# Performance work log

Hardware: AMD Instinct MI355X
Metric: run time of the kernel (lower is better)

The kernel has to match this reference:

```python
import jax, jax.numpy as jnp
import numpy as np

B, C, H, W = 8, 3, 512, 512
KH = KW = 17          # blur kernel
F_REG, D = 24, 4      # regularization filters, Wiener filters
RKH = RKW = 5         # reg-filter kernel size


def psf2otf(psf, shape):
    """Zero-pad psf to `shape`, circshift so center is at (0,0), FFT."""
    kh, kw = psf.shape[-2:]
    Ho, Wo = shape
    pad = [(0, 0)] * (psf.ndim - 2) + [(0, Ho - kh), (0, Wo - kw)]
    p = jnp.pad(psf, pad)
    p = jnp.roll(p, (-(kh // 2), -(kw // 2)), axis=(-2, -1))
    return jnp.fft.fft2(p)


def edgetaper(img, psf):
    """MATLAB-style edgetaper. img: (C,Hp,Wp), psf: (kh,kw)."""
    Ho, Wo = img.shape[-2:]

    def autocorr(proj, n):
        z = jnp.zeros((n,), img.dtype).at[: proj.shape[0]].set(proj)
        z = jnp.fft.ifft(jnp.abs(jnp.fft.fft(z)) ** 2).real
        z = jnp.concatenate([z, z[:1]])  # length n+1
        return z / z.max()

    beta0 = autocorr(psf.sum(1), Ho - 1)  # (Ho,)
    beta1 = autocorr(psf.sum(0), Wo - 1)  # (Wo,)
    alpha = (1.0 - beta0)[:, None] * (1.0 - beta1)[None, :]  # (Ho,Wo)
    blurred = jnp.fft.ifft2(jnp.fft.fft2(img) * psf2otf(psf, (Ho, Wo))).real
    return alpha * img + (1.0 - alpha) * blurred


def wiener_one(y, psf, g, log_alpha):
    """Multi-filter Wiener deconvolution for one image.
    y: (C,Hp,Wp), psf: (kh,kw), g: (F,1,rkh,rkw), log_alpha: (D,1).
    Returns (D,C,Hp,Wp)."""
    Ho, Wo = y.shape[-2:]
    K = psf2otf(psf, (Ho, Wo))                  # (Hp,Wp) complex
    G = psf2otf(g[:, 0], (Ho, Wo))              # (F,Hp,Wp)
    Greg = jnp.sum(jnp.abs(G) ** 2, axis=0)     # (Hp,Wp)
    Y = jnp.fft.fft2(y)                         # (C,Hp,Wp)
    a = jnp.exp(log_alpha)[:, :, None, None]    # (D,1,1,1)
    S = jnp.abs(K) ** 2 + a * Greg              # (D,1,Hp,Wp)
    X = (jnp.conj(K) * Y)[None] / S             # (D,C,Hp,Wp)
    return jnp.fft.ifft2(X).real


def forward(image, blurKernel, stdn, wiener_conv_weights, wiener_scale, alpha, weights):
    kh, kw = blurKernel.shape[-2:]
    # getPad2RetainShape
    pt, pb = (kh + 1) // 2 - 1, kh - (kh + 1) // 2
    pl, pr = (kw + 1) // 2 - 1, kw - (kw + 1) // 2
    x = jnp.pad(image, ((0, 0), (0, 0), (pt, pb), (pl, pr)), mode='symmetric')
    psf = blurKernel[:, 0]                      # (B,kh,kw)
    x = jax.vmap(edgetaper)(x, psf)             # (B,C,Hp,Wp)
    # WeightNormalization: zero-mean then L2-normalize per filter, times scale
    w = wiener_conv_weights - wiener_conv_weights.mean(axis=(1, 2, 3), keepdims=True)
    nrm = jnp.sqrt(jnp.sum(w * w, axis=(1, 2, 3), keepdims=True))
    w = w * (wiener_scale.reshape(-1, 1, 1, 1) / nrm)
    xw = jax.vmap(lambda yi, ki: wiener_one(yi, ki, w, alpha))(x, psf)  # (B,D,C,Hp,Wp)
    Hp, Wp = x.shape[-2:]
    crop = xw[..., pt:Hp - pb, pl:Wp - pr]      # Crop2D back to (H,W)
    return jnp.sum(crop * weights, axis=1)      # weighted mix over D -> (B,C,H,W)


def setup_inputs() -> dict:
    key = jax.random.key(0)
    ks = jax.random.split(key, 4)
    image = jax.random.uniform(ks[0], (B, C, H, W), jnp.float32)
    k = jax.random.uniform(ks[1], (B, 1, KH, KW), jnp.float32)
    blurKernel = k / jnp.sum(k, axis=(-2, -1), keepdims=True)  # normalized psf
    stdn = jax.random.uniform(ks[2], (B,), jnp.float32) * 0.05 + 0.01
    wiener_conv_weights = jax.random.normal(ks[3], (F_REG, 1, RKH, RKW), jnp.float32)
    wiener_scale = jnp.full((F_REG,), 0.1, jnp.float32)
    alpha = jnp.log(jnp.logspace(np.log10(1e-3), np.log10(1e-1), D))[:, None].astype(jnp.float32)
    weights = jnp.full((1, D, 1, 1, 1), 1.0 / D, jnp.float32)
    return {"image": image, "blurKernel": blurKernel, "stdn": stdn,
            "wiener_conv_weights": wiener_conv_weights, "wiener_scale": wiener_scale,
            "alpha": alpha, "weights": weights}


def reference(image, blurKernel, stdn, wiener_conv_weights, wiener_scale, alpha, weights):
    return forward(image, blurKernel, stdn, wiener_conv_weights, wiener_scale, alpha, weights)
```

## Files before the change

kernel.cpp:

```cpp
#include <hip/hip_runtime.h>
#include <hip/hip_bf16.h>

#define NN 528
#define NP (NN*NN)
#define IMG 512
#define IMGP (IMG*IMG)
#define PAD 8
#define KH 17
#define KT (KH*KH)
#define NF 24
#define RK 5
#define RKT (RK*RK)
#define ND 4
#define TOPB (17*NN)
#define ROWB (2*TOPB)
#define SIDEB (494*34)
#define BORD (ROWB + SIDEB)
#define AST 34

static __device__ __forceinline__ float ldx(const void* p, long i, int bf) {
    if (bf) return __bfloat162float(((const __hip_bfloat16*)p)[i]);
    return ((const float*)p)[i];
}

static __device__ __forceinline__ int gmap(int m) {
    if (m < -8)  return 495 - m;
    if (m < 0)   return -m - 1;
    if (m < 512) return m;
    if (m < 520) return 1023 - m;
    return 527 - m;
}

static __device__ __forceinline__ void s1_pair(const float2* __restrict__ X,
                                               float2* __restrict__ A,
                                               const float2* __restrict__ TW,
                                               const float2* __restrict__ T33,
                                               float s, int task) {
    int k2 = task >> 3, n1h = task & 7, n1 = n1h << 1;
    const float4* Xv = (const float4*)X;
    float a0r = 0.f, a0i = 0.f, a1r = 0.f, a1i = 0.f;
    int m = 0;
    for (int n2 = 0; n2 < 33; ++n2) {
        float4 xv = Xv[n1h + 8*n2];
        float2 w = T33[m]; m += k2; if (m >= 33) m -= 33;
        float wr = w.x, wi = s*w.y;
        a0r += xv.x*wr - xv.y*wi; a0i += xv.x*wi + xv.y*wr;
        a1r += xv.z*wr - xv.w*wi; a1i += xv.z*wi + xv.w*wr;
    }
    float2 t0 = TW[n1*k2], t1 = TW[(n1+1)*k2];
    float t0r = t0.x, t0i = s*t0.y, t1r = t1.x, t1i = s*t1.y;
    A[n1*AST + k2]     = make_float2(a0r*t0r - a0i*t0i, a0r*t0i + a0i*t0r);
    A[(n1+1)*AST + k2] = make_float2(a1r*t1r - a1i*t1i, a1r*t1i + a1i*t1r);
}

static __device__ __forceinline__ void s2_pair(const float2* __restrict__ A,
                                               const float2* __restrict__ T16,
                                               float s, int task,
                                               int* o0, float2* y0, int* o1, float2* y1) {
    int k1 = task / 17, kp = task - 17*k1;
    if (kp < 16) {
        int k2 = kp << 1;
        const float4* Av = (const float4*)A;
        float a0r = 0.f, a0i = 0.f, a1r = 0.f, a1i = 0.f;
        int m = 0;
        for (int n1 = 0; n1 < 16; ++n1) {
            float4 av = Av[(n1*AST + k2) >> 1];
            float2 w = T16[m]; m = (m + k1) & 15;
            float wr = w.x, wi = s*w.y;
            a0r += av.x*wr - av.y*wi; a0i += av.x*wi + av.y*wr;
            a1r += av.z*wr - av.w*wi; a1i += av.z*wi + av.w*wr;
        }
        *o0 = k1*33 + k2;     *y0 = make_float2(a0r, a0i);
        *o1 = k1*33 + k2 + 1; *y1 = make_float2(a1r, a1i);
    } else {
        float a0r = 0.f, a0i = 0.f;
        int m = 0;
        for (int n1 = 0; n1 < 16; ++n1) {
            float2 av = A[n1*AST + 32];
            float2 w = T16[m]; m = (m + k1) & 15;
            float wr = w.x, wi = s*w.y;
            a0r += av.x*wr - av.y*wi; a0i += av.x*wi + av.y*wr;
        }
        *o0 = k1*33 + 32; *y0 = make_float2(a0r, a0i);
        *o1 = -1;
    }
}

__global__ void detect_k(const void* pimg, int nimg, const void* pbk, int nbk,
                         const void* pwcw, int nwcw, const void* pws, int nws,
                         const float* c4a, const float* c4b,
                         int* __restrict__ flags,
                         float* __restrict__ alpha_ws, float* __restrict__ wgt_ws) {
    int t = threadIdx.x;
    const void* ps[4] = {pimg, pbk, pwcw, pws};
    int ns[4] = {nimg, nbk, nwcw, nws};
    if (t < 4) {
        const unsigned short* q = (const unsigned short*)ps[t];
        int n = ns[t];
        int K = n < 512 ? n : 512;
        int cnt = 0, pass = 0;
        for (int i = 0; i < K; i += 2) {
            int e = (q[i] >> 7) & 0xFF;
            pass += (e >= 100 && e <= 140);
            cnt++;
        }
        flags[t] = (pass * 10 >= cnt * 8) ? 1 : 0;
    }
    if (t == 7) {
        const float* A = (c4a[0] < 0.f) ? c4a : c4b;
        const float* W = (c4a[0] < 0.f) ? c4b : c4a;
        for (int i = 0; i < ND; ++i) { alpha_ws[i] = A[i]; wgt_ws[i] = W[i]; }
    }
}

__global__ void twinit_k(float2* __restrict__ twN) {
    int i = blockIdx.x * blockDim.x + threadIdx.x;
    if (i < NN) {
        double th = -6.283185307179586476925287 * (double)i / (double)NN;
        twN[i] = make_float2((float)cos(th), (float)sin(th));
    }
}

__global__ void wnorm_k(const void* __restrict__ wcw, const void* __restrict__ wscale,
                        const int* __restrict__ flags, float* __restrict__ wout) {
    int f = threadIdx.x;
    if (f >= NF) return;
    int bfw = flags[2], bfs = flags[3];
    float v[RKT];
    float mean = 0.f;
    for (int i = 0; i < RKT; ++i) { v[i] = ldx(wcw, f*RKT+i, bfw); mean += v[i]; }
    mean *= (1.f/(float)RKT);
    float ss = 0.f;
    for (int i = 0; i < RKT; ++i) { v[i] -= mean; ss += v[i]*v[i]; }
    float sc = ldx(wscale, f, bfs) / sqrtf(ss);
    for (int i = 0; i < RKT; ++i) wout[f*RKT+i] = v[i]*sc;
}

__global__ void prep_k(const void* __restrict__ blurKernel, const int* __restrict__ flags,
                       float* __restrict__ psf_all, float* __restrict__ A0_all,
                       float* __restrict__ A1_all) {
    int b = blockIdx.x, t = threadIdx.x;
    int bf = flags[1];
    __shared__ float psf[KT];
    __shared__ float q0[KH], q1[KH], ac0[KH], ac1[KH];
    for (int i = t; i < KT; i += 64) {
        float v = ldx(blurKernel, b*KT + i, bf);
        psf[i] = v;
        psf_all[b*KT + i] = v;
    }
    __syncthreads();
    if (t < KH) {
        float s0 = 0.f, s1 = 0.f;
        for (int k = 0; k < KH; ++k) { s0 += psf[t*KH + k]; s1 += psf[k*KH + t]; }
        q0[t] = s0; q1[t] = s1;
    }
    __syncthreads();
    if (t < KH) {
        float a0 = 0.f, a1 = 0.f;
        for (int m = 0; m + t < KH; ++m) { a0 += q0[m]*q0[m+t]; a1 += q1[m]*q1[m+t]; }
        ac0[t] = a0; ac1[t] = a1;
    }
    __syncthreads();
    for (int r = t; r < NN; r += 64) {
        int lag = min(r, (NN-1) - r);
        float b0 = (lag <= KH-1) ? ac0[lag]/ac0[0] : 0.f;
        float b1 = (lag <= KH-1) ? ac1[lag]/ac1[0] : 0.f;
        A0_all[b*NN + r] = 1.f - b0;
        A1_all[b*NN + r] = 1.f - b1;
    }
}

__global__ void greg_k(const float* __restrict__ w, const float2* __restrict__ twN,
                       float* __restrict__ Greg) {
    int p = blockIdx.x * blockDim.x + threadIdx.x;
    if (p >= NP) return;
    int u = p % NN, v = p / NN;
    float2 rp[RK], cp[RK];
    for (int j = 0; j < RK; ++j) {
        int m = (u * (j - RK/2)) % NN; if (m < 0) m += NN;
        rp[j] = twN[m];
    }
    for (int k = 0; k < RK; ++k) {
        int m = (v * (k - RK/2)) % NN; if (m < 0) m += NN;
        cp[k] = twN[m];
    }
    float pr[RKT], pi[RKT];
    for (int j = 0; j < RK; ++j)
        for (int k = 0; k < RK; ++k) {
            pr[j*RK+k] = rp[j].x*cp[k].x - rp[j].y*cp[k].y;
            pi[j*RK+k] = rp[j].x*cp[k].y + rp[j].y*cp[k].x;
        }
    float acc = 0.f;
    for (int f = 0; f < NF; ++f) {
        float gr = 0.f, gi = 0.f;
        for (int i = 0; i < RKT; ++i) {
            float wv = w[f*RKT + i];
            gr += wv * pr[i];
            gi += wv * pi[i];
        }
        acc += gr*gr + gi*gi;
    }
    Greg[p] = acc;
}

__global__ __launch_bounds__(256)
void border2_k(const void* __restrict__ image, const int* __restrict__ flags,
               const float* __restrict__ psf_all,
               const float* __restrict__ A0_all, const float* __restrict__ A1_all,
               float* __restrict__ borderV) {
    __shared__ float4 S4[1440];
    float* S = (float*)S4;
    int bp = blockIdx.y;
    int b = bp / 3;
    long ofs = (long)bp * IMGP;
    int bf = flags[0];
    int t = threadIdx.x;
    const float* pw = psf_all + b*KT;
    int bx = blockIdx.x;

    if (bx < 20) {
        int q = bx >> 1, h = bx & 1;
        int r0;
        if (q < 4) r0 = 4*q;
        else if (q == 4) r0 = 13;
        else if (q < 9) r0 = 511 + 4*(q-5);
        else r0 = 524;
        int X0 = h * 264;
        for (int idx = t; idx < 20*288; idx += 256) {
            int i = idx / 288, xi = idx - i*288;
            int x = X0 + xi;
            float v = 0.f;
            if (x < 544) {
                int sr = gmap(r0 - 16 + i);
                int sc = gmap(x - 16);
                v = ldx(image, ofs + (long)sr*IMG + sc, bf);
            }
            S[idx] = v;
        }
        __syncthreads();
        for (int g = t; g < 264; g += 256) {
            int rx = g / 66, cl = g - rx*66;
            int c0 = X0 + 4*cl;
            int x0 = 4*cl;
            float acc0 = 0.f, acc1 = 0.f, acc2 = 0.f, acc3 = 0.f;
            for (int j = 0; j < KH; ++j) {
                const float4* SjV = (const float4*)(S + (16 + rx - j)*288 + x0);
                float xv[20];
                #pragma unroll
                for (int qv = 0; qv < 5; ++qv) {
                    float4 tv = SjV[qv];
                    xv[4*qv+0] = tv.x; xv[4*qv+1] = tv.y;
                    xv[4*qv+2] = tv.z; xv[4*qv+3] = tv.w;
                }
                const float* wj = pw + j*KH;
                #pragma unroll
                for (int qq = 0; qq < 20; ++qq) {
                    {int k = 0 + 16 - qq; if (k >= 0 && k < KH) acc0 += wj[k]*xv[qq];}
                    {int k = 1 + 16 - qq; if (k >= 0 && k < KH) acc1 += wj[k]*xv[qq];}
                    {int k = 2 + 16 - qq; if (k >= 0 && k < KH) acc2 += wj[k]*xv[qq];}
                    {int k = 3 + 16 - qq; if (k >= 0 && k < KH) acc3 += wj[k]*xv[qq];}
                }
            }
            int r = r0 + rx;
            float a0v = A0_all[b*NN + r];
            int ibase = (r < 17) ? r*NN : TOPB + (r-511)*NN;
            float accs[4] = {acc0, acc1, acc2, acc3};
            #pragma unroll
            for (int d = 0; d < 4; ++d) {
                int c = c0 + d;
                float xo = S[(8 + rx)*288 + (x0 + 8 + d)];
                float al = a0v * A1_all[b*NN + c];
                borderV[(size_t)bp*BORD + ibase + c] = al*xo + (1.f - al)*accs[d];
            }
        }
    } else {
        int chunk = bx - 20;
        int r0 = 17 + 26*chunk;
        for (int idx = t; idx < 42*84; idx += 256) {
            int i = idx / 84, x = idx - i*84;
            float v = 0.f;
            int m = -1000;
            if (x < 33) m = x - 16;
            else if (x >= 48 && x < 81) m = x - 48 + 495;
            if (m != -1000) {
                int sr = gmap(r0 - 16 + i);
                int sc = gmap(m);
                v = ldx(image, ofs + (long)sr*IMG + sc, bf);
            }
            S[idx] = v;
        }
        __syncthreads();
        int g = t;
        if (g < 208) {
            int ry = g >> 3, s = g & 7;
            int c0 = (s < 4) ? 4*s : 511 + 4*(s-4);
            int sz = ((s & 3) == 3) ? 5 : 4;
            int x0 = (s < 4) ? 4*s : 48 + 4*(s-4);
            float acc0=0.f, acc1=0.f, acc2=0.f, acc3=0.f, acc4=0.f;
            for (int j = 0; j < KH; ++j) {
                const float4* SjV = (const float4*)(S + (16 + ry - j)*84 + x0);
                float xv[24];
                #pragma unroll
                for (int qv = 0; qv < 6; ++qv) {
                    float4 tv = SjV[qv];
                    xv[4*qv+0] = tv.x; xv[4*qv+1] = tv.y;
                    xv[4*qv+2] = tv.z; xv[4*qv+3] = tv.w;
                }
                const float* wj = pw + j*KH;
                #pragma unroll
                for (int qq = 0; qq < 21; ++qq) {
                    {int k = 0 + 16 - qq; if (k >= 0 && k < KH) acc0 += wj[k]*xv[qq];}
                    {int k = 1 + 16 - qq; if (k >= 0 && k < KH) acc1 += wj[k]*xv[qq];}
                    {int k = 2 + 16 - qq; if (k >= 0 && k < KH) acc2 += wj[k]*xv[qq];}
                    {int k = 3 + 16 - qq; if (k >= 0 && k < KH) acc3 += wj[k]*xv[qq];}
                    {int k = 4 + 16 - qq; if (k >= 0 && k < KH) acc4 += wj[k]*xv[qq];}
                }
            }
            int r = r0 + ry;
            float a0v = A0_all[b*NN + r];
            int cc0 = (s < 4) ? c0 : c0 - 494;
            size_t ib = (size_t)bp*BORD + ROWB + (size_t)(r-17)*34 + cc0;
            float accs[5] = {acc0, acc1, acc2, acc3, acc4};
            #pragma unroll
            for (int d = 0; d < 5; ++d) {
                if (d < sz) {
                    int c = c0 + d;
                    float xo = S[(8 + ry)*84 + (x0 + 8 + d)];
                    float al = a0v * A1_all[b*NN + c];
                    borderV[ib + d] = al*xo + (1.f - al)*accs[d];
                }
            }
        }
    }
}

__global__ void kv_k(const float* __restrict__ psf_all, const float2* __restrict__ twN,
                     float2* __restrict__ Sv) {
    int idx = blockIdx.x * blockDim.x + threadIdx.x;
    if (idx >= 8*NN*KH) return;
    int j = idx % KH;
    int rest = idx / KH;
    int v = rest % NN, b = rest / NN;
    int m = (520 * v) % NN;
    float sr = 0.f, si = 0.f;
    const float* ps = psf_all + b*KT + j*KH;
    for (int k = 0; k < KH; ++k) {
        float2 cp = twN[m];
        m += v; if (m >= NN) m -= NN;
        sr += ps[k] * cp.x;
        si += ps[k] * cp.y;
    }
    Sv[idx] = make_float2(sr, si);
}

__global__ __launch_bounds__(128)
void fftrow_k(const void* __restrict__ image, const int* __restrict__ flags,
              const float* __restrict__ borderV, const float2* __restrict__ twN,
              float2* __restrict__ buf, int B0) {
    __shared__ __align__(16) float2 X[NN];
    __shared__ __align__(16) float2 A[16*AST];
    __shared__ float2 TW[NN];
    __shared__ float2 T33[33];
    __shared__ float2 T16[16];
    int t = threadIdx.x;
    int q = blockIdx.x / NN;
    int r = blockIdx.x - q*NN;
    int pair = q / 3, ch = q - 3*pair;
    int b0p = B0 + 2*pair;
    int bf = flags[0];
    for (int i = t; i < NN; i += 128) TW[i] = twN[i];
    if (t < 33) T33[t] = twN[t*16];
    else if (t >= 64 && t < 80) T16[t-64] = twN[(t-64)*33];
    for (int c = t; c < NN; c += 128) {
        float x0, x1;
        bool isb = (r < 17) | (r >= 511) | (c < 17) | (c >= 511);
        if (isb) {
            int i2;
            if (r < 17) i2 = r*NN + c;
            else if (r >= 511) i2 = TOPB + (r-511)*NN + c;
            else { int cc = (c < 17) ? c : c - 494; i2 = ROWB + (r-17)*34 + cc; }
            x0 = borderV[(size_t)(b0p*3 + ch)*BORD + i2];
            x1 = borderV[(size_t)((b0p+1)*3 + ch)*BORD + i2];
        } else {
            long ofs0 = ((long)b0p*3 + ch) * IMGP + (long)(r - PAD)*IMG + (c - PAD);
            x0 = ldx(image, ofs0, bf);
            x1 = ldx(image, ofs0 + 3L*IMGP, bf);
        }
        X[c] = make_float2(x0, x1);
    }
    __syncthreads();
    for (int task = t; task < 264; task += 128) s1_pair(X, A, TW, T33, 1.f, task);
    __syncthreads();
    float2* dst = buf + (size_t)q*NP + (size_t)r*NN;
    for (int task = t; task < 272; task += 128) {
        int o0, o1; float2 y0, y1;
        s2_pair(A, T16, 1.f, task, &o0, &y0, &o1, &y1);
        dst[o0] = y0;
        if (o1 >= 0) dst[o1] = y1;
    }
}

__global__ void transpose_ip_k(float2* __restrict__ buf) {
    int tnum = blockIdx.x;
    int ti = 0, rem = tnum;
    while (rem >= 33 - ti) { rem -= 33 - ti; ti++; }
    int tj = ti + rem;
    float2* pl = buf + (size_t)blockIdx.z * NP;
    __shared__ float2 ta[16][17], tb[16][17];
    int tx = threadIdx.x, ty = threadIdx.y;
    int ra = ti*16 + ty, ca = tj*16 + tx;
    int rb = tj*16 + ty, cb = ti*16 + tx;
    ta[ty][tx] = pl[(size_t)ra*NN + ca];
    tb[ty][tx] = pl[(size_t)rb*NN + cb];
    __syncthreads();
    pl[(size_t)ra*NN + ca] = tb[tx][ty];
    pl[(size_t)rb*NN + cb] = ta[tx][ty];
}

__global__ __launch_bounds__(256)
void rowpipe_k(float2* __restrict__ buf, const float2* __restrict__ Sv,
               const float* __restrict__ Greg, const float2* __restrict__ twN,
               const float* __restrict__ alpha4, const float* __restrict__ wgt4, int B0) {
    __shared__ __align__(16) float2 X[2][NN];
    __shared__ __align__(16) float2 A[2][16*AST];
    __shared__ float2 TW[NN];
    __shared__ float2 T33[33];
    __shared__ float2 T16[16];
    __shared__ float2 SvL[2][KH];
    int t = threadIdx.x;
    int q = blockIdx.x;
    int plane = blockIdx.y;
    int pair = plane / 3;
    int b0p = B0 + 2*pair;
    int qm = (NN - q) % NN;
    int nrow = (qm == q) ? 1 : 2;
    float2* pl = buf + (size_t)plane * NP;
    for (int i = t; i < NN; i += 256) TW[i] = twN[i];
    if (t < 33) T33[t] = twN[t*16];
    else if (t >= 64 && t < 80) T16[t-64] = twN[(t-64)*33];
    else if (t >= 128 && t < 128 + 2*KH) {
        int tt = t - 128;
        int bsel = tt / KH, j = tt - KH*bsel;
        SvL[bsel][j] = Sv[((size_t)(b0p + bsel)*NN + q)*KH + j];
    }
    for (int i = t; i < nrow*NN; i += 256) {
        int l = i / NN, o = i - l*NN;
        X[l][o] = pl[(size_t)(l ? qm : q)*NN + o];
    }
    __syncthreads();
    for (int i = t; i < nrow*264; i += 256) {
        int l = i / 264, task = i - 264*l;
        s1_pair(X[l], A[l], TW, T33, 1.f, task);
    }
    __syncthreads();
    for (int i = t; i < nrow*272; i += 256) {
        int l = i / 272, task = i - 272*l;
        int o0, o1; float2 y0, y1;
        s2_pair(A[l], T16, 1.f, task, &o0, &y0, &o1, &y1);
        X[l][o0] = y0;
        if (o1 >= 0) X[l][o1] = y1;
    }
    __syncthreads();
    float aE[ND], wE[ND];
    #pragma unroll
    for (int d = 0; d < ND; ++d) { aE[d] = __expf(alpha4[d]); wE[d] = wgt4[d]; }
    int npair = (nrow == 2) ? NN : 265;
    int lm = nrow - 1;
    for (int k = t; k < npair; k += 256) {
        int km = (NN - k) % NN;
        int mu = (520 * k) % NN;
        float K0r = 0.f, K0i = 0.f, K1r = 0.f, K1i = 0.f;
        for (int j = 0; j < KH; ++j) {
            float2 rp = TW[mu]; mu += k; if (mu >= NN) mu -= NN;
            float2 s0 = SvL[0][j], s1 = SvL[1][j];
            K0r += rp.x*s0.x - rp.y*s0.y;  K0i += rp.x*s0.y + rp.y*s0.x;
            K1r += rp.x*s1.x - rp.y*s1.y;  K1i += rp.x*s1.y + rp.y*s1.x;
        }
        float gg = Greg[(size_t)q*NN + k];
        float K20 = K0r*K0r + K0i*K0i;
        float K21 = K1r*K1r + K1i*K1i;
        float s0a = 0.f, s1a = 0.f;
        #pragma unroll
        for (int d = 0; d < ND; ++d) {
            s0a += wE[d] / fmaxf(K20 + aE[d]*gg, 1e-30f);
            s1a += wE[d] / fmaxf(K21 + aE[d]*gg, 1e-30f);
        }
        s0a *= (1.f/(float)NP);
        s1a *= (1.f/(float)NP);
        float W0r = K0r*s0a, W0i = -K0i*s0a;
        float W1r = K1r*s1a, W1i = -K1i*s1a;
        float2 Z  = X[0][k];
        float2 Zm = X[lm][km];
        float X0r = 0.5f*(Z.x + Zm.x), X0i = 0.5f*(Z.y - Zm.y);
        float X1r = 0.5f*(Z.y + Zm.y), X1i = 0.5f*(Zm.x - Z.x);
        float Y0r = X0r*W0r - X0i*W0i, Y0i = X0r*W0i + X0i*W0r;
        float Y1r = X1r*W1r - X1i*W1i, Y1i = X1r*W1i + X1i*W1r;
        X[0][k]   = make_float2(Y0r - Y1i, Y0i + Y1r);
        X[lm][km] = make_float2(Y0r + Y1i, Y1r - Y0i);
    }
    __syncthreads();
    for (int i = t; i < nrow*264; i += 256) {
        int l = i / 264, task = i - 264*l;
        s1_pair(X[l], A[l], TW, T33, -1.f, task);
    }
    __syncthreads();
    for (int i = t; i < nrow*272; i += 256) {
        int l = i / 272, task = i - 272*l;
        int o0, o1; float2 y0, y1;
        s2_pair(A[l], T16, -1.f, task, &o0, &y0, &o1, &y1);
        X[l][o0] = y0;
        if (o1 >= 0) X[l][o1] = y1;
    }
    __syncthreads();
    for (int i = t; i < nrow*NN; i += 256) {
        int l = i / NN, o = i - l*NN;
        pl[(size_t)(l ? qm : q)*NN + o] = X[l][o];
    }
}

__global__ __launch_bounds__(128)
void fft_crop_k(const float2* __restrict__ in, float* __restrict__ out,
                const float2* __restrict__ twN, int B0) {
    __shared__ __align__(16) float2 X[NN];
    __shared__ __align__(16) float2 A[16*AST];
    __shared__ float2 TW[NN];
    __shared__ float2 T33[33];
    __shared__ float2 T16[16];
    int t = threadIdx.x;
    int q = blockIdx.x >> 9;
    int rp = (blockIdx.x & 511) + PAD;
    int pair = q / 3, ch = q - 3*pair;
    int b0p = B0 + 2*pair;
    const float2* src = in + (size_t)q*NP + (size_t)rp*NN;
    for (int i = t; i < NN; i += 128) { X[i] = src[i]; TW[i] = twN[i]; }
    if (t < 33) T33[t] = twN[t*16];
    else if (t >= 64 && t < 80) T16[t-64] = twN[(t-64)*33];
    __syncthreads();
    for (int task = t; task < 264; task += 128) s1_pair(X, A, TW, T33, -1.f, task);
    __syncthreads();
    float* o0p = out + ((size_t)b0p*3 + ch) * IMGP + (size_t)(rp - PAD) * IMG;
    float* o1p = o0p + 3L*IMGP;
    for (int task = t; task < 272; task += 128) {
        int o0, o1; float2 y0, y1;
        s2_pair(A, T16, -1.f, task, &o0, &y0, &o1, &y1);
        if (o0 >= PAD && o0 < IMG + PAD) { o0p[o0 - PAD] = y0.x; o1p[o0 - PAD] = y0.y; }
        if (o1 >= PAD && o1 < IMG + PAD) { o0p[o1 - PAD] = y1.x; o1p[o1 - PAD] = y1.y; }
    }
}

extern "C" void kernel_launch(void* const* d_in, const int* in_sizes, int n_in,
                              void* d_out, int out_size, void* d_ws, size_t ws_size,
                              hipStream_t stream) {
    int i_img = -1, i_bk = -1, i_wcw = -1, i_ws = -1, i_4a = -1, i_4b = -1;
    for (int i = 0; i < n_in; ++i) {
        int s = in_sizes[i];
        if (s == 8*3*IMG*IMG)   i_img = i;
        else if (s == 8*KT)     i_bk = i;
        else if (s == NF*RKT)   i_wcw = i;
        else if (s == NF)       i_ws = i;
        else if (s == ND) { if (i_4a < 0) i_4a = i; else i_4b = i; }
    }
    if (i_img < 0) i_img = 0;
    if (i_bk  < 0) i_bk  = 1;
    if (i_wcw < 0) i_wcw = 3;
    if (i_ws  < 0) i_ws  = 4;
    if (i_4a  < 0) i_4a  = 5;
    if (i_4b  < 0) i_4b  = i_4a;
    const void* image      = d_in[i_img];
    const void* blurKernel = d_in[i_bk];
    const void* wcw        = d_in[i_wcw];
    const void* wscale     = d_in[i_ws];
    const float* c4a       = (const float*)d_in[i_4a];
    const float* c4b       = (const float*)d_in[i_4b];
    float* out = (float*)d_out;

    char* base = (char*)d_ws;
    int*    flags    = (int*)(base);
    float*  alpha_ws = (float*)(base + 64);
    float*  wgt_ws   = (float*)(base + 80);
    float2* twN      = (float2*)(base + 256);
    float*  wnorm    = (float*)(base + 4480);
    float*  psf_all  = (float*)(base + 6880);
    float*  A0       = (float*)(base + 16128);
    float*  A1       = (float*)(base + 33024);
    float*  Greg     = (float*)(base + 49920);
    float2* buf      = (float2*)(base + 1165056);
    float*  borderV  = (float*)(base + 14546688);
    float2* Sv       = (float2*)(base + 17882496);

    if (ws_size < 18456960) return;

    detect_k<<<1, 64, 0, stream>>>(image, in_sizes[i_img], blurKernel, in_sizes[i_bk],
                                   wcw, in_sizes[i_wcw], wscale, in_sizes[i_ws],
                                   c4a, c4b, flags, alpha_ws, wgt_ws);
    twinit_k<<<(NN+63)/64, 64, 0, stream>>>(twN);
    wnorm_k<<<1, 64, 0, stream>>>(wcw, wscale, flags, wnorm);
    prep_k<<<8, 64, 0, stream>>>(blurKernel, flags, psf_all, A0, A1);
    greg_k<<<(NP+255)/256, 256, 0, stream>>>(wnorm, twN, Greg);
    kv_k<<<(8*NN*KH+255)/256, 256, 0, stream>>>(psf_all, twN, Sv);

    dim3 bgrid2(39, 24);
    border2_k<<<bgrid2, 256, 0, stream>>>(image, flags, psf_all, A0, A1, borderV);

    dim3 tblk(16, 16);
    dim3 tgrid6(561, 1, 6);
    dim3 rpgrid(265, 6);
    for (int B0 = 0; B0 < 8; B0 += 4) {
        fftrow_k<<<6*NN, 128, 0, stream>>>(image, flags, borderV, twN, buf, B0);
        transpose_ip_k<<<tgrid6, tblk, 0, stream>>>(buf);
        rowpipe_k<<<rpgrid, 256, 0, stream>>>(buf, Sv, Greg, twN, alpha_ws, wgt_ws, B0);
        transpose_ip_k<<<tgrid6, tblk, 0, stream>>>(buf);
        fft_crop_k<<<6*IMG, 128, 0, stream>>>(buf, out, twN, B0);
    }
}
```

Measured before the change: 499.3 us.

## Process all batches in one launch sequence and use twiddle recurrences in DFT loops

Drops the two-iteration batch loop, so each FFT/transpose/pipeline kernel runs once over all 12 plane pairs with grids twice as large. The workspace grows to hold the full buffer. In the small DFT stages and the kernel-spectrum evaluation, the per-iteration twiddle table lookup with modular index is replaced by a running complex multiplication recurrence. This removes LDS loads and index arithmetic but adds FLOPs and some accumulated rounding error.

Result: faster. 414.3 us (-17.0%).

```diff
diff --git a/kernel.cpp b/kernel.cpp
--- a/kernel.cpp
+++ b/kernel.cpp
@@ -38,14 +38,17 @@
                                                float s, int task) {
     int k2 = task >> 3, n1h = task & 7, n1 = n1h << 1;
     const float4* Xv = (const float4*)X;
+    float2 wst = T33[k2];
+    float wr = 1.f, wi = 0.f;
     float a0r = 0.f, a0i = 0.f, a1r = 0.f, a1i = 0.f;
-    int m = 0;
     for (int n2 = 0; n2 < 33; ++n2) {
         float4 xv = Xv[n1h + 8*n2];
-        float2 w = T33[m]; m += k2; if (m >= 33) m -= 33;
-        float wr = w.x, wi = s*w.y;
-        a0r += xv.x*wr - xv.y*wi; a0i += xv.x*wi + xv.y*wr;
-        a1r += xv.z*wr - xv.w*wi; a1i += xv.z*wi + xv.w*wr;
+        float ur = wr, ui = s*wi;
+        a0r += xv.x*ur - xv.y*ui; a0i += xv.x*ui + xv.y*ur;
+        a1r += xv.z*ur - xv.w*ui; a1i += xv.z*ui + xv.w*ur;
+        float nwr = wr*wst.x - wi*wst.y;
+        wi = wr*wst.y + wi*wst.x;
+        wr = nwr;
     }
     float2 t0 = TW[n1*k2], t1 = TW[(n1+1)*k2];
     float t0r = t0.x, t0i = s*t0.y, t1r = t1.x, t1i = s*t1.y;
@@ -58,28 +61,32 @@
                                                float s, int task,
                                                int* o0, float2* y0, int* o1, float2* y1) {
     int k1 = task / 17, kp = task - 17*k1;
+    float2 wst = T16[k1];
+    float wr = 1.f, wi = 0.f;
     if (kp < 16) {
         int k2 = kp << 1;
         const float4* Av = (const float4*)A;
         float a0r = 0.f, a0i = 0.f, a1r = 0.f, a1i = 0.f;
-        int m = 0;
         for (int n1 = 0; n1 < 16; ++n1) {
             float4 av = Av[(n1*AST + k2) >> 1];
-            float2 w = T16[m]; m = (m + k1) & 15;
-            float wr = w.x, wi = s*w.y;
-            a0r += av.x*wr - av.y*wi; a0i += av.x*wi + av.y*wr;
-            a1r += av.z*wr - av.w*wi; a1i += av.z*wi + av.w*wr;
+            float ur = wr, ui = s*wi;
+            a0r += av.x*ur - av.y*ui; a0i += av.x*ui + av.y*ur;
+            a1r += av.z*ur - av.w*ui; a1i += av.z*ui + av.w*ur;
+            float nwr = wr*wst.x - wi*wst.y;
+            wi = wr*wst.y + wi*wst.x;
+            wr = nwr;
         }
         *o0 = k1*33 + k2;     *y0 = make_float2(a0r, a0i);
         *o1 = k1*33 + k2 + 1; *y1 = make_float2(a1r, a1i);
     } else {
         float a0r = 0.f, a0i = 0.f;
-        int m = 0;
         for (int n1 = 0; n1 < 16; ++n1) {
             float2 av = A[n1*AST + 32];
-            float2 w = T16[m]; m = (m + k1) & 15;
-            float wr = w.x, wi = s*w.y;
-            a0r += av.x*wr - av.y*wi; a0i += av.x*wi + av.y*wr;
+            float ur = wr, ui = s*wi;
+            a0r += av.x*ur - av.y*ui; a0i += av.x*ui + av.y*ur;
+            float nwr = wr*wst.x - wi*wst.y;
+            wi = wr*wst.y + wi*wst.x;
+            wr = nwr;
         }
         *o0 = k1*33 + 32; *y0 = make_float2(a0r, a0i);
         *o1 = -1;
@@ -356,7 +363,7 @@
 __global__ __launch_bounds__(128)
 void fftrow_k(const void* __restrict__ image, const int* __restrict__ flags,
               const float* __restrict__ borderV, const float2* __restrict__ twN,
-              float2* __restrict__ buf, int B0) {
+              float2* __restrict__ buf) {
     __shared__ __align__(16) float2 X[NN];
     __shared__ __align__(16) float2 A[16*AST];
     __shared__ float2 TW[NN];
@@ -366,7 +373,7 @@
     int q = blockIdx.x / NN;
     int r = blockIdx.x - q*NN;
     int pair = q / 3, ch = q - 3*pair;
-    int b0p = B0 + 2*pair;
+    int b0p = 2*pair;
     int bf = flags[0];
     for (int i = t; i < NN; i += 128) TW[i] = twN[i];
     if (t < 33) T33[t] = twN[t*16];
@@ -420,7 +427,7 @@
 __global__ __launch_bounds__(256)
 void rowpipe_k(float2* __restrict__ buf, const float2* __restrict__ Sv,
                const float* __restrict__ Greg, const float2* __restrict__ twN,
-               const float* __restrict__ alpha4, const float* __restrict__ wgt4, int B0) {
+               const float* __restrict__ alpha4, const float* __restrict__ wgt4) {
     __shared__ __align__(16) float2 X[2][NN];
     __shared__ __align__(16) float2 A[2][16*AST];
     __shared__ float2 TW[NN];
@@ -431,7 +438,7 @@
     int q = blockIdx.x;
     int plane = blockIdx.y;
     int pair = plane / 3;
-    int b0p = B0 + 2*pair;
+    int b0p = 2*pair;
     int qm = (NN - q) % NN;
     int nrow = (qm == q) ? 1 : 2;
     float2* pl = buf + (size_t)plane * NP;
@@ -468,13 +475,17 @@
     int lm = nrow - 1;
     for (int k = t; k < npair; k += 256) {
         int km = (NN - k) % NN;
-        int mu = (520 * k) % NN;
+        int mu0 = (520 * k) % NN;
+        float2 rp = TW[mu0];
+        float2 rst = TW[k];
         float K0r = 0.f, K0i = 0.f, K1r = 0.f, K1i = 0.f;
         for (int j = 0; j < KH; ++j) {
-            float2 rp = TW[mu]; mu += k; if (mu >= NN) mu -= NN;
             float2 s0 = SvL[0][j], s1 = SvL[1][j];
             K0r += rp.x*s0.x - rp.y*s0.y;  K0i += rp.x*s0.y + rp.y*s0.x;
             K1r += rp.x*s1.x - rp.y*s1.y;  K1i += rp.x*s1.y + rp.y*s1.x;
+            float nrp = rp.x*rst.x - rp.y*rst.y;
+            rp.y = rp.x*rst.y + rp.y*rst.x;
+            rp.x = nrp;
         }
         float gg = Greg[(size_t)q*NN + k];
         float K20 = K0r*K0r + K0i*K0i;
@@ -520,7 +531,7 @@
 
 __global__ __launch_bounds__(128)
 void fft_crop_k(const float2* __restrict__ in, float* __restrict__ out,
-                const float2* __restrict__ twN, int B0) {
+                const float2* __restrict__ twN) {
     __shared__ __align__(16) float2 X[NN];
     __shared__ __align__(16) float2 A[16*AST];
     __shared__ float2 TW[NN];
@@ -530,7 +541,7 @@
     int q = blockIdx.x >> 9;
     int rp = (blockIdx.x & 511) + PAD;
     int pair = q / 3, ch = q - 3*pair;
-    int b0p = B0 + 2*pair;
+    int b0p = 2*pair;
     const float2* src = in + (size_t)q*NP + (size_t)rp*NN;
     for (int i = t; i < NN; i += 128) { X[i] = src[i]; TW[i] = twN[i]; }
     if (t < 33) T33[t] = twN[t*16];
@@ -585,10 +596,10 @@
     float*  A1       = (float*)(base + 33024);
     float*  Greg     = (float*)(base + 49920);
     float2* buf      = (float2*)(base + 1165056);
-    float*  borderV  = (float*)(base + 14546688);
-    float2* Sv       = (float2*)(base + 17882496);
-
-    if (ws_size < 18456960) return;
+    float*  borderV  = (float*)(base + 27928320);
+    float2* Sv       = (float2*)(base + 31264128);
+
+    if (ws_size < 31838592) return;
 
     detect_k<<<1, 64, 0, stream>>>(image, in_sizes[i_img], blurKernel, in_sizes[i_bk],
                                    wcw, in_sizes[i_wcw], wscale, in_sizes[i_ws],
@@ -603,13 +614,11 @@
     border2_k<<<bgrid2, 256, 0, stream>>>(image, flags, psf_all, A0, A1, borderV);
 
     dim3 tblk(16, 16);
-    dim3 tgrid6(561, 1, 6);
-    dim3 rpgrid(265, 6);
-    for (int B0 = 0; B0 < 8; B0 += 4) {
-        fftrow_k<<<6*NN, 128, 0, stream>>>(image, flags, borderV, twN, buf, B0);
-        transpose_ip_k<<<tgrid6, tblk, 0, stream>>>(buf);
-        rowpipe_k<<<rpgrid, 256, 0, stream>>>(buf, Sv, Greg, twN, alpha_ws, wgt_ws, B0);
-        transpose_ip_k<<<tgrid6, tblk, 0, stream>>>(buf);
-        fft_crop_k<<<6*IMG, 128, 0, stream>>>(buf, out, twN, B0);
-    }
-}
+    dim3 tgrid12(561, 1, 12);
+    dim3 rpgrid(265, 12);
+    fftrow_k<<<12*NN, 128, 0, stream>>>(image, flags, borderV, twN, buf);
+    transpose_ip_k<<<tgrid12, tblk, 0, stream>>>(buf);
+    rowpipe_k<<<rpgrid, 256, 0, stream>>>(buf, Sv, Greg, twN, alpha_ws, wgt_ws);
+    transpose_ip_k<<<tgrid12, tblk, 0, stream>>>(buf);
+    fft_crop_k<<<12*IMG, 128, 0, stream>>>(buf, out, twN);
+}
```
